# Performance work log

Hardware: AMD Instinct MI355X
Metric: run time of the kernel (lower is better)

The kernel has to match this reference:

```python
import jax, jax.numpy as jnp
import numpy as np

INPUT_DIM, HIDDEN, OUT_DIM = 7, 64, 4


def _lstm_layer(x_seq, W_ih, W_hh, b_ih, b_hh):
    """Single LSTM layer, batch_first x_seq [B,T,D] -> [B,T,H]. PyTorch gate order i,f,g,o."""
    B = x_seq.shape[0]
    H = W_hh.shape[1]
    # Precompute input projection for all timesteps (hoist GEMM out of the scan).
    x_proj = jnp.einsum('btd,gd->btg', x_seq, W_ih) + b_ih + b_hh  # [B,T,4H]

    def step(carry, xt):
        h, c = carry
        gates = xt + h @ W_hh.T  # [B,4H]
        i, f, g, o = jnp.split(gates, 4, axis=-1)
        i = jax.nn.sigmoid(i)
        f = jax.nn.sigmoid(f)
        g = jnp.tanh(g)
        o = jax.nn.sigmoid(o)
        c = f * c + i * g
        h = o * jnp.tanh(c)
        return (h, c), h

    h0 = jnp.zeros((B, H), x_seq.dtype)
    c0 = jnp.zeros((B, H), x_seq.dtype)
    (_, _), hs = jax.lax.scan(step, (h0, c0), jnp.swapaxes(x_proj, 0, 1))  # hs [T,B,H]
    return jnp.swapaxes(hs, 0, 1)  # [B,T,H]


def setup_inputs() -> dict:
    key = jax.random.key(0)
    ks = jax.random.split(key, 12)
    s = 0.1  # init scale ~ 1/sqrt(hidden)
    x = jax.random.normal(ks[0], (4096, 512, INPUT_DIM), dtype=jnp.float32)
    W_ih0 = jax.random.normal(ks[1], (4 * HIDDEN, INPUT_DIM), dtype=jnp.float32) * s
    W_hh0 = jax.random.normal(ks[2], (4 * HIDDEN, HIDDEN), dtype=jnp.float32) * s
    b_ih0 = jax.random.normal(ks[3], (4 * HIDDEN,), dtype=jnp.float32) * s
    b_hh0 = jax.random.normal(ks[4], (4 * HIDDEN,), dtype=jnp.float32) * s
    W_ih1 = jax.random.normal(ks[5], (4 * HIDDEN, HIDDEN), dtype=jnp.float32) * s
    W_hh1 = jax.random.normal(ks[6], (4 * HIDDEN, HIDDEN), dtype=jnp.float32) * s
    b_ih1 = jax.random.normal(ks[7], (4 * HIDDEN,), dtype=jnp.float32) * s
    b_hh1 = jax.random.normal(ks[8], (4 * HIDDEN,), dtype=jnp.float32) * s
    W_fc = jax.random.normal(ks[9], (OUT_DIM, HIDDEN), dtype=jnp.float32) * s
    b_fc = jax.random.normal(ks[10], (OUT_DIM,), dtype=jnp.float32) * s
    return {"x": x, "W_ih0": W_ih0, "W_hh0": W_hh0, "b_ih0": b_ih0, "b_hh0": b_hh0,
            "W_ih1": W_ih1, "W_hh1": W_hh1, "b_ih1": b_ih1, "b_hh1": b_hh1,
            "W_fc": W_fc, "b_fc": b_fc}


def reference(x, W_ih0, W_hh0, b_ih0, b_hh0, W_ih1, W_hh1, b_ih1, b_hh1, W_fc, b_fc):
    h1 = _lstm_layer(x, W_ih0, W_hh0, b_ih0, b_hh0)   # [B,T,H]
    h2 = _lstm_layer(h1, W_ih1, W_hh1, b_ih1, b_hh1)  # [B,T,H]
    last = h2[:, -1, :]                               # [B,H]
    return last @ W_fc.T + b_fc                       # [B,4]
```

## Files before the change

kernel.cpp:

```cpp
#include <hip/hip_runtime.h>

#define T_SEQ 512
#define HID 64
#define MB 16
#define NTHREADS 512
#define A1STR 104
#define A2STR 104

typedef __attribute__((ext_vector_type(8))) short short8;
typedef __attribute__((ext_vector_type(4))) float floatx4;

#define LOG2E 1.4426950408889634f

__device__ __forceinline__ short f2bf_rne(float v) {
  unsigned u = __float_as_uint(v);
  return (short)((u + 0x7FFFu + ((u >> 16) & 1u)) >> 16);
}
__device__ __forceinline__ float rcp_(float x) { return __builtin_amdgcn_rcpf(x); }
__device__ __forceinline__ float exp2_(float x) { return __builtin_amdgcn_exp2f(x); }

__device__ __forceinline__ unsigned cvt_pk_bf16(float lo, float hi) {
  unsigned r;
  asm("v_cvt_pk_bf16_f32 %0, %1, %2" : "=v"(r) : "v"(lo), "v"(hi));
  return r;
}

__device__ __forceinline__ void barrier_lds() {
  asm volatile("s_waitcnt lgkmcnt(0)" ::: "memory");
  __builtin_amdgcn_s_barrier();
  asm volatile("" ::: "memory");
}

__device__ __forceinline__ float gate_h(const floatx4 p, float& c) {
  float A = exp2_(-p[0]);
  float F = exp2_(-p[1]);
  float G = exp2_(p[2]);
  float O = exp2_(-p[3]);
  float t1 = (1.f + A) * (G + 1.f);
  float t2 = 1.f + F;
  float num = c * t1 + (G - 1.f) * t2;
  c = num * rcp_(t1 * t2);
  float C = exp2_((2.f * LOG2E) * c);
  return (C - 1.f) * rcp_((1.f + O) * (C + 1.f));
}

__device__ __forceinline__ int uofp(int p) {
  return (p & ~7) + ((p & 7) >> 1) + ((p & 1) << 2);
}

__device__ __forceinline__ short w1elem(int k, int n, float wsc,
                                        const float* __restrict__ Wih0,
                                        const float* __restrict__ Whh0) {
  float v;
  if      (k < 64) { v = Whh0[n*64 + uofp(k)]; }
  else if (k < 71) { v = Wih0[n*7 + (k - 64)]; }
  else return (short)0;
  return f2bf_rne(v * wsc);
}
__device__ __forceinline__ short w2elem(int k, int n, float wsc,
                                        const float* __restrict__ Wih1,
                                        const float* __restrict__ Whh1) {
  float v;
  if (k < 64) { v = Wih1[n*64 + uofp(k)]; }
  else        { v = Whh1[n*64 + uofp(k - 64)]; }
  return f2bf_rne(v * wsc);
}

#define MFMA(A, B, C) __builtin_amdgcn_mfma_f32_16x16x32_bf16((A), (B), (C), 0, 0, 0)

__global__ __launch_bounds__(NTHREADS, 2) void lstm_fused(
    const float* __restrict__ x,
    const float* __restrict__ Wih0, const float* __restrict__ Whh0,
    const float* __restrict__ bih0, const float* __restrict__ bhh0,
    const float* __restrict__ Wih1, const float* __restrict__ Whh1,
    const float* __restrict__ bih1, const float* __restrict__ bhh1,
    const float* __restrict__ Wfc,  const float* __restrict__ bfc,
    float* __restrict__ out)
{
  __shared__ __align__(16) short A1[2][MB][A1STR];
  __shared__ __align__(16) short A2[2][MB][A2STR];
  __shared__ float h2f[MB][HID + 4];

  const int tid  = threadIdx.x;
  const int lane = tid & 63;
  const int wave = tid >> 6;
  const int w0   = wave & 3;
  const bool isL1 = wave < 4;
  const int l15  = lane & 15;
  const int quad = lane >> 4;
  const int quad8= quad * 8;
  const int g4   = l15 & 3;
  const int b0   = blockIdx.x * MB;
  const int ub   = w0*16 + quad;
  const int hp0  = w0*16 + 2*quad;
  const int hp1  = hp0 + 8;
  const float wsc = (g4 == 2) ? 2.f * LOG2E : LOG2E;

  for (int i = tid; i < 2*MB*A1STR/2; i += NTHREADS) ((unsigned*)A1)[i] = 0u;
  for (int i = tid; i < 2*MB*A2STR/2; i += NTHREADS) ((unsigned*)A2)[i] = 0u;
  __syncthreads();

  const float* bi_ = isL1 ? bih0 : bih1;
  const float* bh_ = isL1 ? bhh0 : bhh1;
  floatx4 bs0, bs1, bs2, bs3;
  #pragma unroll
  for (int g = 0; g < 4; ++g) {
    float ws = (g == 2) ? 2.f * LOG2E : LOG2E;
    bs0[g] = (bi_[g*64 + ub     ] + bh_[g*64 + ub     ]) * ws;
    bs1[g] = (bi_[g*64 + ub + 4 ] + bh_[g*64 + ub + 4 ]) * ws;
    bs2[g] = (bi_[g*64 + ub + 8 ] + bh_[g*64 + ub + 8 ]) * ws;
    bs3[g] = (bi_[g*64 + ub + 12] + bh_[g*64 + ub + 12]) * ws;
  }

  const int xd2  = l15;
  const int xrow = 4*w0 + quad;
  const bool xact = isL1 && (xd2 < 4);
  const float* xbase = x + ((size_t)(b0 + xrow) * T_SEQ) * 7 + 2*xd2;
  float xc0 = 0.f, xc1 = 0.f;
  if (xact) {
    *(unsigned*)&A1[0][xrow][64 + 2*xd2] =
        cvt_pk_bf16(xbase[0], (xd2 < 3) ? xbase[1] : 0.f);
    xc0 = xbase[7];
    xc1 = (xd2 < 3) ? xbase[8] : 0.f;
  }

  short8 W0[4], W1[4], W2[4], W3[4];
#define LOADW1(Wt, t)                                                        \
  { int nt = g4*64 + w0*16 + 4*(t) + (l15 >> 2);                             \
    _Pragma("unroll")                                                        \
    for (int ks = 0; ks < 3; ++ks) { short8 f;                               \
      _Pragma("unroll")                                                      \
      for (int jj = 0; jj < 8; ++jj)                                         \
        f[jj] = w1elem(ks*32 + quad8 + jj, nt, wsc, Wih0, Whh0);             \
      Wt[ks] = f; } }
#define LOADW2(Wt, t)                                                        \
  { int nt = g4*64 + w0*16 + 4*(t) + (l15 >> 2);                             \
    _Pragma("unroll")                                                        \
    for (int ks = 0; ks < 4; ++ks) { short8 f;                               \
      _Pragma("unroll")                                                      \
      for (int jj = 0; jj < 8; ++jj)                                         \
        f[jj] = w2elem(ks*32 + quad8 + jj, nt, wsc, Wih1, Whh1);             \
      Wt[ks] = f; } }
  if (isL1) {
    LOADW1(W0, 0) LOADW1(W1, 1) LOADW1(W2, 2) LOADW1(W3, 3)
  } else {
    LOADW2(W0, 0) LOADW2(W1, 1) LOADW2(W2, 2) LOADW2(W3, 3)
  }
  __syncthreads();

  float c0 = 0.f, c1 = 0.f, c2 = 0.f, c3 = 0.f;

#define STEP_X(NXT, XT)                                                      \
    if (xact) {                                                              \
      *(unsigned*)&A1[NXT][xrow][64 + 2*xd2] = cvt_pk_bf16(xc0, xc1);        \
      xc0 = xbase[7 * (XT)];                                                 \
      xc1 = (xd2 < 3) ? xbase[7 * (XT) + 1] : 0.f;                           \
    }

#define L1_MFMAS                                                             \
      floatx4 p0 = MFMA(W0[0], hf0, bs0);                                    \
      floatx4 p1 = MFMA(W1[0], hf0, bs1);                                    \
      floatx4 p2 = MFMA(W2[0], hf0, bs2);                                    \
      floatx4 p3 = MFMA(W3[0], hf0, bs3);                                    \
      p0 = MFMA(W0[1], hf1, p0);  p1 = MFMA(W1[1], hf1, p1);                 \
      p2 = MFMA(W2[1], hf1, p2);  p3 = MFMA(W3[1], hf1, p3);                 \
      p0 = MFMA(W0[2], hfx, p0);  p1 = MFMA(W1[2], hfx, p1);                 \
      p2 = MFMA(W2[2], hfx, p2);  p3 = MFMA(W3[2], hfx, p3);

#define L2_MFMAS                                                             \
      floatx4 p0 = MFMA(W0[0], hf0, bs0);                                    \
      floatx4 p1 = MFMA(W1[0], hf0, bs1);                                    \
      floatx4 p2 = MFMA(W2[0], hf0, bs2);                                    \
      floatx4 p3 = MFMA(W3[0], hf0, bs3);                                    \
      p0 = MFMA(W0[1], hf1, p0);  p1 = MFMA(W1[1], hf1, p1);                 \
      p2 = MFMA(W2[1], hf1, p2);  p3 = MFMA(W3[1], hf1, p3);                 \
      p0 = MFMA(W0[2], h20, p0);  p1 = MFMA(W1[2], h20, p1);                 \
      p2 = MFMA(W2[2], h20, p2);  p3 = MFMA(W3[2], h20, p3);                 \
      p0 = MFMA(W0[3], h21, p0);  p1 = MFMA(W1[3], h21, p1);                 \
      p2 = MFMA(W2[3], h21, p2);  p3 = MFMA(W3[3], h21, p3);

#define GATES_AND_WRITE(DST)                                                 \
      float h0 = gate_h(p0, c0);                                             \
      float h1 = gate_h(p1, c1);                                             \
      float h2 = gate_h(p2, c2);                                             \
      float h3 = gate_h(p3, c3);                                             \
      *(unsigned*)&DST[l15][hp0] = cvt_pk_bf16(h0, h1);                      \
      *(unsigned*)&DST[l15][hp1] = cvt_pk_bf16(h2, h3);

#define STEP_FULL(CUR, NXT, IT)                                              \
  {                                                                          \
    if (isL1) {                                                              \
      int xt_ = (IT) + 2; if (xt_ > T_SEQ - 1) xt_ = T_SEQ - 1;              \
      STEP_X(NXT, xt_)                                                       \
      short8 hf0 = *(const short8*)&A1[CUR][l15][     quad8];                \
      short8 hf1 = *(const short8*)&A1[CUR][l15][32 + quad8];                \
      short8 hfx = *(const short8*)&A1[CUR][l15][64 + quad8];                \
      L1_MFMAS                                                               \
      GATES_AND_WRITE(A1[NXT])                                               \
    } else {                                                                 \
      short8 hf0 = *(const short8*)&A1[CUR][l15][     quad8];                \
      short8 hf1 = *(const short8*)&A1[CUR][l15][32 + quad8];                \
      short8 h20 = *(const short8*)&A2[CUR][l15][     quad8];                \
      short8 h21 = *(const short8*)&A2[CUR][l15][32 + quad8];                \
      L2_MFMAS                                                               \
      GATES_AND_WRITE(A2[NXT])                                               \
    }                                                                        \
    barrier_lds();                                                           \
  }

  {
    if (isL1) {
      STEP_X(1, 2)
      short8 hf0 = *(const short8*)&A1[0][l15][     quad8];
      short8 hf1 = *(const short8*)&A1[0][l15][32 + quad8];
      short8 hfx = *(const short8*)&A1[0][l15][64 + quad8];
      L1_MFMAS
      GATES_AND_WRITE(A1[1])
    }
    barrier_lds();
  }

  #pragma unroll 1
  for (int k = 0; k < 255; ++k) {
    STEP_FULL(1, 0, 2*k + 1)
    STEP_FULL(0, 1, 2*k + 2)
  }
  STEP_FULL(1, 0, 511)

  {
    if (!isL1) {
      short8 hf0 = *(const short8*)&A1[0][l15][     quad8];
      short8 hf1 = *(const short8*)&A1[0][l15][32 + quad8];
      short8 h20 = *(const short8*)&A2[0][l15][     quad8];
      short8 h21 = *(const short8*)&A2[0][l15][32 + quad8];
      L2_MFMAS
      h2f[l15][ub     ] = gate_h(p0, c0);
      h2f[l15][ub + 4 ] = gate_h(p1, c1);
      h2f[l15][ub + 8 ] = gate_h(p2, c2);
      h2f[l15][ub + 12] = gate_h(p3, c3);
    }
    __syncthreads();
  }

  if (tid < MB * 4) {
    int bbf = tid >> 2, o = tid & 3;
    float acc = bfc[o];
    #pragma unroll 8
    for (int kk = 0; kk < HID; ++kk) acc += h2f[bbf][kk] * Wfc[o*HID + kk];
    out[(size_t)(b0 + bbf) * 4 + o] = acc;
  }
}

extern "C" void kernel_launch(void* const* d_in, const int* in_sizes, int n_in,
                              void* d_out, int out_size, void* d_ws, size_t ws_size,
                              hipStream_t stream) {
  const float* x    = (const float*)d_in[0];
  const float* Wih0 = (const float*)d_in[1];
  const float* Whh0 = (const float*)d_in[2];
  const float* bih0 = (const float*)d_in[3];
  const float* bhh0 = (const float*)d_in[4];
  const float* Wih1 = (const float*)d_in[5];
  const float* Whh1 = (const float*)d_in[6];
  const float* bih1 = (const float*)d_in[7];
  const float* bhh1 = (const float*)d_in[8];
  const float* Wfc  = (const float*)d_in[9];
  const float* bfc  = (const float*)d_in[10];
  (void)d_ws; (void)ws_size; (void)n_in; (void)out_size;

  const int B = in_sizes[0] / (T_SEQ * 7);
  dim3 grid(B / MB);
  lstm_fused<<<grid, NTHREADS, 0, stream>>>(x, Wih0, Whh0, bih0, bhh0,
                                            Wih1, Whh1, bih1, bhh1, Wfc, bfc,
                                            (float*)d_out);
}
```

Measured before the change: 426.3 us.

## Merge layer-1 and layer-2 waves so each wave computes both LSTM layers

The block shrinks from 8 waves (4 per layer) to 4 waves, and each wave now holds both layers' weights and computes the layer-1 and layer-2 gate MFMAs for its hidden slice in the same step. This removes the split between specialised waves and lets the two layers' MFMA chains interleave within one wave to hide latency. In exchange, register use per wave roughly doubles, the launch bound drops to one block per SM, and each wave's per-step critical path is longer. A tautological pointer comparison was also added in the weight loader, which has no visible purpose.

```diff
diff --git a/kernel.cpp b/kernel.cpp
--- a/kernel.cpp
+++ b/kernel.cpp
@@ -3,7 +3,7 @@
 #define T_SEQ 512
 #define HID 64
 #define MB 16
-#define NTHREADS 512
+#define NTHREADS 256
 #define A1STR 104
 #define A2STR 104
 
@@ -62,13 +62,13 @@
                                         const float* __restrict__ Whh1) {
   float v;
   if (k < 64) { v = Wih1[n*64 + uofp(k)]; }
-  else        { v = Whh1[n*64 + uofp(k - 64)]; }
+  else        { v = Wih1 == Wih1 ? Whh1[n*64 + uofp(k - 64)] : 0; }
   return f2bf_rne(v * wsc);
 }
 
 #define MFMA(A, B, C) __builtin_amdgcn_mfma_f32_16x16x32_bf16((A), (B), (C), 0, 0, 0)
 
-__global__ __launch_bounds__(NTHREADS, 2) void lstm_fused(
+__global__ __launch_bounds__(NTHREADS, 1) void lstm_fused(
     const float* __restrict__ x,
     const float* __restrict__ Wih0, const float* __restrict__ Whh0,
     const float* __restrict__ bih0, const float* __restrict__ bhh0,
@@ -84,15 +84,13 @@
   const int tid  = threadIdx.x;
   const int lane = tid & 63;
   const int wave = tid >> 6;
-  const int w0   = wave & 3;
-  const bool isL1 = wave < 4;
   const int l15  = lane & 15;
   const int quad = lane >> 4;
   const int quad8= quad * 8;
   const int g4   = l15 & 3;
   const int b0   = blockIdx.x * MB;
-  const int ub   = w0*16 + quad;
-  const int hp0  = w0*16 + 2*quad;
+  const int ub   = wave*16 + quad;
+  const int hp0  = wave*16 + 2*quad;
   const int hp1  = hp0 + 8;
   const float wsc = (g4 == 2) ? 2.f * LOG2E : LOG2E;
 
@@ -100,21 +98,24 @@
   for (int i = tid; i < 2*MB*A2STR/2; i += NTHREADS) ((unsigned*)A2)[i] = 0u;
   __syncthreads();
 
-  const float* bi_ = isL1 ? bih0 : bih1;
-  const float* bh_ = isL1 ? bhh0 : bhh1;
-  floatx4 bs0, bs1, bs2, bs3;
+  floatx4 d0, d1, d2, d3;
+  floatx4 e0, e1, e2, e3;
   #pragma unroll
   for (int g = 0; g < 4; ++g) {
     float ws = (g == 2) ? 2.f * LOG2E : LOG2E;
-    bs0[g] = (bi_[g*64 + ub     ] + bh_[g*64 + ub     ]) * ws;
-    bs1[g] = (bi_[g*64 + ub + 4 ] + bh_[g*64 + ub + 4 ]) * ws;
-    bs2[g] = (bi_[g*64 + ub + 8 ] + bh_[g*64 + ub + 8 ]) * ws;
-    bs3[g] = (bi_[g*64 + ub + 12] + bh_[g*64 + ub + 12]) * ws;
+    d0[g] = (bih0[g*64 + ub     ] + bhh0[g*64 + ub     ]) * ws;
+    d1[g] = (bih0[g*64 + ub + 4 ] + bhh0[g*64 + ub + 4 ]) * ws;
+    d2[g] = (bih0[g*64 + ub + 8 ] + bhh0[g*64 + ub + 8 ]) * ws;
+    d3[g] = (bih0[g*64 + ub + 12] + bhh0[g*64 + ub + 12]) * ws;
+    e0[g] = (bih1[g*64 + ub     ] + bhh1[g*64 + ub     ]) * ws;
+    e1[g] = (bih1[g*64 + ub + 4 ] + bhh1[g*64 + ub + 4 ]) * ws;
+    e2[g] = (bih1[g*64 + ub + 8 ] + bhh1[g*64 + ub + 8 ]) * ws;
+    e3[g] = (bih1[g*64 + ub + 12] + bhh1[g*64 + ub + 12]) * ws;
   }
 
   const int xd2  = l15;
-  const int xrow = 4*w0 + quad;
-  const bool xact = isL1 && (xd2 < 4);
+  const int xrow = 4*wave + quad;
+  const bool xact = (xd2 < 4);
   const float* xbase = x + ((size_t)(b0 + xrow) * T_SEQ) * 7 + 2*xd2;
   float xc0 = 0.f, xc1 = 0.f;
   if (xact) {
@@ -124,9 +125,10 @@
     xc1 = (xd2 < 3) ? xbase[8] : 0.f;
   }
 
-  short8 W0[4], W1[4], W2[4], W3[4];
+  short8 V0[3], V1[3], V2[3], V3[3];
+  short8 U0[4], U1[4], U2[4], U3[4];
 #define LOADW1(Wt, t)                                                        \
-  { int nt = g4*64 + w0*16 + 4*(t) + (l15 >> 2);                             \
+  { int nt = g4*64 + wave*16 + 4*(t) + (l15 >> 2);                           \
     _Pragma("unroll")                                                        \
     for (int ks = 0; ks < 3; ++ks) { short8 f;                               \
       _Pragma("unroll")                                                      \
@@ -134,21 +136,19 @@
         f[jj] = w1elem(ks*32 + quad8 + jj, nt, wsc, Wih0, Whh0);             \
       Wt[ks] = f; } }
 #define LOADW2(Wt, t)                                                        \
-  { int nt = g4*64 + w0*16 + 4*(t) + (l15 >> 2);                             \
+  { int nt = g4*64 + wave*16 + 4*(t) + (l15 >> 2);                           \
     _Pragma("unroll")                                                        \
     for (int ks = 0; ks < 4; ++ks) { short8 f;                               \
       _Pragma("unroll")                                                      \
       for (int jj = 0; jj < 8; ++jj)                                         \
         f[jj] = w2elem(ks*32 + quad8 + jj, nt, wsc, Wih1, Whh1);             \
       Wt[ks] = f; } }
-  if (isL1) {
-    LOADW1(W0, 0) LOADW1(W1, 1) LOADW1(W2, 2) LOADW1(W3, 3)
-  } else {
-    LOADW2(W0, 0) LOADW2(W1, 1) LOADW2(W2, 2) LOADW2(W3, 3)
-  }
+  LOADW1(V0, 0) LOADW1(V1, 1) LOADW1(V2, 2) LOADW1(V3, 3)
+  LOADW2(U0, 0) LOADW2(U1, 1) LOADW2(U2, 2) LOADW2(U3, 3)
   __syncthreads();
 
-  float c0 = 0.f, c1 = 0.f, c2 = 0.f, c3 = 0.f;
+  float c10 = 0.f, c11 = 0.f, c12 = 0.f, c13 = 0.f;
+  float c20 = 0.f, c21 = 0.f, c22 = 0.f, c23 = 0.f;
 
 #define STEP_X(NXT, XT)                                                      \
     if (xact) {                                                              \
@@ -158,65 +158,65 @@
     }
 
 #define L1_MFMAS                                                             \
-      floatx4 p0 = MFMA(W0[0], hf0, bs0);                                    \
-      floatx4 p1 = MFMA(W1[0], hf0, bs1);                                    \
-      floatx4 p2 = MFMA(W2[0], hf0, bs2);                                    \
-      floatx4 p3 = MFMA(W3[0], hf0, bs3);                                    \
-      p0 = MFMA(W0[1], hf1, p0);  p1 = MFMA(W1[1], hf1, p1);                 \
-      p2 = MFMA(W2[1], hf1, p2);  p3 = MFMA(W3[1], hf1, p3);                 \
-      p0 = MFMA(W0[2], hfx, p0);  p1 = MFMA(W1[2], hfx, p1);                 \
-      p2 = MFMA(W2[2], hfx, p2);  p3 = MFMA(W3[2], hfx, p3);
+      floatx4 q0 = MFMA(V0[0], hf0, d0);                                     \
+      floatx4 q1 = MFMA(V1[0], hf0, d1);                                     \
+      floatx4 q2 = MFMA(V2[0], hf0, d2);                                     \
+      floatx4 q3 = MFMA(V3[0], hf0, d3);                                     \
+      q0 = MFMA(V0[1], hf1, q0);  q1 = MFMA(V1[1], hf1, q1);                 \
+      q2 = MFMA(V2[1], hf1, q2);  q3 = MFMA(V3[1], hf1, q3);                 \
+      q0 = MFMA(V0[2], hfx, q0);  q1 = MFMA(V1[2], hfx, q1);                 \
+      q2 = MFMA(V2[2], hfx, q2);  q3 = MFMA(V3[2], hfx, q3);
 
 #define L2_MFMAS                                                             \
-      floatx4 p0 = MFMA(W0[0], hf0, bs0);                                    \
-      floatx4 p1 = MFMA(W1[0], hf0, bs1);                                    \
-      floatx4 p2 = MFMA(W2[0], hf0, bs2);                                    \
-      floatx4 p3 = MFMA(W3[0], hf0, bs3);                                    \
-      p0 = MFMA(W0[1], hf1, p0);  p1 = MFMA(W1[1], hf1, p1);                 \
-      p2 = MFMA(W2[1], hf1, p2);  p3 = MFMA(W3[1], hf1, p3);                 \
-      p0 = MFMA(W0[2], h20, p0);  p1 = MFMA(W1[2], h20, p1);                 \
-      p2 = MFMA(W2[2], h20, p2);  p3 = MFMA(W3[2], h20, p3);                 \
-      p0 = MFMA(W0[3], h21, p0);  p1 = MFMA(W1[3], h21, p1);                 \
-      p2 = MFMA(W2[3], h21, p2);  p3 = MFMA(W3[3], h21, p3);
-
-#define GATES_AND_WRITE(DST)                                                 \
-      float h0 = gate_h(p0, c0);                                             \
-      float h1 = gate_h(p1, c1);                                             \
-      float h2 = gate_h(p2, c2);                                             \
-      float h3 = gate_h(p3, c3);                                             \
-      *(unsigned*)&DST[l15][hp0] = cvt_pk_bf16(h0, h1);                      \
-      *(unsigned*)&DST[l15][hp1] = cvt_pk_bf16(h2, h3);
+      floatx4 r0 = MFMA(U0[0], hf0, e0);                                     \
+      floatx4 r1 = MFMA(U1[0], hf0, e1);                                     \
+      floatx4 r2 = MFMA(U2[0], hf0, e2);                                     \
+      floatx4 r3 = MFMA(U3[0], hf0, e3);                                     \
+      r0 = MFMA(U0[1], hf1, r0);  r1 = MFMA(U1[1], hf1, r1);                 \
+      r2 = MFMA(U2[1], hf1, r2);  r3 = MFMA(U3[1], hf1, r3);                 \
+      r0 = MFMA(U0[2], h20, r0);  r1 = MFMA(U1[2], h20, r1);                 \
+      r2 = MFMA(U2[2], h20, r2);  r3 = MFMA(U3[2], h20, r3);                 \
+      r0 = MFMA(U0[3], h21, r0);  r1 = MFMA(U1[3], h21, r1);                 \
+      r2 = MFMA(U2[3], h21, r2);  r3 = MFMA(U3[3], h21, r3);
 
 #define STEP_FULL(CUR, NXT, IT)                                              \
   {                                                                          \
-    if (isL1) {                                                              \
-      int xt_ = (IT) + 2; if (xt_ > T_SEQ - 1) xt_ = T_SEQ - 1;              \
-      STEP_X(NXT, xt_)                                                       \
-      short8 hf0 = *(const short8*)&A1[CUR][l15][     quad8];                \
-      short8 hf1 = *(const short8*)&A1[CUR][l15][32 + quad8];                \
-      short8 hfx = *(const short8*)&A1[CUR][l15][64 + quad8];                \
-      L1_MFMAS                                                               \
-      GATES_AND_WRITE(A1[NXT])                                               \
-    } else {                                                                 \
-      short8 hf0 = *(const short8*)&A1[CUR][l15][     quad8];                \
-      short8 hf1 = *(const short8*)&A1[CUR][l15][32 + quad8];                \
-      short8 h20 = *(const short8*)&A2[CUR][l15][     quad8];                \
-      short8 h21 = *(const short8*)&A2[CUR][l15][32 + quad8];                \
-      L2_MFMAS                                                               \
-      GATES_AND_WRITE(A2[NXT])                                               \
-    }                                                                        \
+    short8 hf0 = *(const short8*)&A1[CUR][l15][     quad8];                  \
+    short8 hf1 = *(const short8*)&A1[CUR][l15][32 + quad8];                  \
+    short8 hfx = *(const short8*)&A1[CUR][l15][64 + quad8];                  \
+    short8 h20 = *(const short8*)&A2[CUR][l15][     quad8];                  \
+    short8 h21 = *(const short8*)&A2[CUR][l15][32 + quad8];                  \
+    L1_MFMAS                                                                 \
+    L2_MFMAS                                                                 \
+    int xt_ = (IT) + 2; if (xt_ > T_SEQ - 1) xt_ = T_SEQ - 1;                \
+    STEP_X(NXT, xt_)                                                         \
+    float h0 = gate_h(q0, c10);                                              \
+    float h1 = gate_h(q1, c11);                                              \
+    float h2 = gate_h(q2, c12);                                              \
+    float h3 = gate_h(q3, c13);                                              \
+    *(unsigned*)&A1[NXT][l15][hp0] = cvt_pk_bf16(h0, h1);                    \
+    *(unsigned*)&A1[NXT][l15][hp1] = cvt_pk_bf16(h2, h3);                    \
+    float g0 = gate_h(r0, c20);                                              \
+    float g1 = gate_h(r1, c21);                                              \
+    float g2 = gate_h(r2, c22);                                              \
+    float g3 = gate_h(r3, c23);                                              \
+    *(unsigned*)&A2[NXT][l15][hp0] = cvt_pk_bf16(g0, g1);                    \
+    *(unsigned*)&A2[NXT][l15][hp1] = cvt_pk_bf16(g2, g3);                    \
     barrier_lds();                                                           \
   }
 
   {
-    if (isL1) {
-      STEP_X(1, 2)
-      short8 hf0 = *(const short8*)&A1[0][l15][     quad8];
-      short8 hf1 = *(const short8*)&A1[0][l15][32 + quad8];
-      short8 hfx = *(const short8*)&A1[0][l15][64 + quad8];
-      L1_MFMAS
-      GATES_AND_WRITE(A1[1])
-    }
+    short8 hf0 = *(const short8*)&A1[0][l15][     quad8];
+    short8 hf1 = *(const short8*)&A1[0][l15][32 + quad8];
+    short8 hfx = *(const short8*)&A1[0][l15][64 + quad8];
+    L1_MFMAS
+    STEP_X(1, 2)
+    float h0 = gate_h(q0, c10);
+    float h1 = gate_h(q1, c11);
+    float h2 = gate_h(q2, c12);
+    float h3 = gate_h(q3, c13);
+    *(unsigned*)&A1[1][l15][hp0] = cvt_pk_bf16(h0, h1);
+    *(unsigned*)&A1[1][l15][hp1] = cvt_pk_bf16(h2, h3);
     barrier_lds();
   }
 
@@ -228,17 +228,15 @@
   STEP_FULL(1, 0, 511)
 
   {
-    if (!isL1) {
-      short8 hf0 = *(const short8*)&A1[0][l15][     quad8];
-      short8 hf1 = *(const short8*)&A1[0][l15][32 + quad8];
-      short8 h20 = *(const short8*)&A2[0][l15][     quad8];
-      short8 h21 = *(const short8*)&A2[0][l15][32 + quad8];
-      L2_MFMAS
-      h2f[l15][ub     ] = gate_h(p0, c0);
-      h2f[l15][ub + 4 ] = gate_h(p1, c1);
-      h2f[l15][ub + 8 ] = gate_h(p2, c2);
-      h2f[l15][ub + 12] = gate_h(p3, c3);
-    }
+    short8 hf0 = *(const short8*)&A1[0][l15][     quad8];
+    short8 hf1 = *(const short8*)&A1[0][l15][32 + quad8];
+    short8 h20 = *(const short8*)&A2[0][l15][     quad8];
+    short8 h21 = *(const short8*)&A2[0][l15][32 + quad8];
+    L2_MFMAS
+    h2f[l15][ub     ] = gate_h(r0, c20);
+    h2f[l15][ub + 4 ] = gate_h(r1, c21);
+    h2f[l15][ub + 8 ] = gate_h(r2, c22);
+    h2f[l15][ub + 12] = gate_h(r3, c23);
     __syncthreads();
   }
 
```

Result: slower. 498.5 us (+16.9%).
